# Kernel tuning notes

Measured on AMD Instinct MI355X. Metric: run time of the kernel, lower is better.

## Reference

```python
import jax, jax.numpy as jnp
import numpy as np

P = 2  # sampling ratio: keep top ceil(M/p) measurements


def setup_inputs() -> dict:
    key = jax.random.key(0)
    k1, k2, k3 = jax.random.split(key, 3)
    B, H, W, C = 8, 1024, 1024, 3
    Y = jax.random.normal(k1, (B, H, W, C), dtype=jnp.float32)
    # build()-time Z0 components: abs ~ N(0.5, 0.1), angle ~ N(0, 0.5*sqrt(pi))
    Z0_abs = 0.5 + 0.1 * jax.random.normal(k2, (1, 1, H, W), dtype=jnp.float32)
    Z0_angle = (0.5 * np.pi ** 0.5) * jax.random.normal(k3, (1, 1, H, W), dtype=jnp.float32)
    return {"Y": Y, "Z0_abs": Z0_abs, "Z0_angle": Z0_angle}


def _make_Z0(Z0_abs, Z0_angle):
    # Z0 = |Z0| * exp(i*angle), Frobenius-normalized over spatial axes (2,3)
    Z0 = Z0_abs.astype(jnp.complex64) * jnp.exp(1j * Z0_angle.astype(jnp.complex64))
    fro = jnp.sqrt(jnp.sum(jnp.abs(Z0) ** 2, axis=(2, 3), keepdims=True)).astype(jnp.complex64)
    return Z0 / fro


def reference(Y, Z0_abs, Z0_angle):
    B, H, W, C = Y.shape
    M = H * W * C
    R = int(np.ceil(M / P))
    # transpose NHWC -> NCHW, scale by original S[2] (= W)
    Y_S = jnp.transpose(Y.astype(jnp.float32), (0, 3, 1, 2)) / jnp.float32(W)
    y_s = Y_S.reshape(B, M)
    # threshold = R-th largest value per batch (== descending-sorted index R-1)
    thr = jax.lax.top_k(y_s, R)[0][:, -1]  # [B]
    Ytr = (Y_S >= thr[:, None, None, None]).astype(jnp.float32)  # [B,C,H,W]
    Z0 = _make_Z0(Z0_abs, Z0_angle)
    return Ytr, Z0
```

## Files before the change

kernel.cpp:

```cpp
#include <hip/hip_runtime.h>
#include <math.h>

#define BATCH 8
#define HH 1024
#define WW 1024
#define CC 3
#define MTOT (HH*WW*CC)
#define RSEL 1572864u

#define WCAP 131072u
#define LCAP 1024u
#define P1B  2048
#define QPT  4

#define U_HI 0xBC800000u
#define U_LO 0x437FFFFFu

typedef float nfloat4 __attribute__((ext_vector_type(4)));
typedef float nfloat2 __attribute__((ext_vector_type(2)));

#define WS_WCNT_OFF  0u
#define WS_CHI_OFF   512u
#define WS_NPART_OFF 1024u
#define WS_THR_OFF   2048u
#define WS_FB_OFF    2112u
#define WS_NORM_OFF  2176u
#define WS_WU_OFF    4096u
#define WS_WP_OFF    4198400u

#define NCOPY 3
#define HSTRIDE 4097

__device__ __forceinline__ unsigned int fmap(float x) {
    unsigned int b = __float_as_uint(x);
    return (b & 0x80000000u) ? ~b : (b | 0x80000000u);
}

__device__ __forceinline__ void nt_store4(float4 v, float4* p) {
    nfloat4 t; t.x = v.x; t.y = v.y; t.z = v.z; t.w = v.w;
    __builtin_nontemporal_store(t, (nfloat4*)p);
}
__device__ __forceinline__ void nt_store2(float2 v, float2* p) {
    nfloat2 t; t.x = v.x; t.y = v.y;
    __builtin_nontemporal_store(t, (nfloat2*)p);
}

__device__ __forceinline__ void thresh_row_quad(const float* __restrict__ Yb,
                                                float* __restrict__ outb,
                                                int h, int w4, unsigned int tu) {
    const float4* src = (const float4*)(Yb + ((size_t)h * WW + (size_t)w4 * 4) * CC);
    float4 a0 = src[0], a1 = src[1], a2 = src[2];
    float4 r0, r1, r2;
    r0.x = (fmap(a0.x) >= tu) ? 1.f : 0.f;
    r0.y = (fmap(a0.w) >= tu) ? 1.f : 0.f;
    r0.z = (fmap(a1.z) >= tu) ? 1.f : 0.f;
    r0.w = (fmap(a2.y) >= tu) ? 1.f : 0.f;
    r1.x = (fmap(a0.y) >= tu) ? 1.f : 0.f;
    r1.y = (fmap(a1.x) >= tu) ? 1.f : 0.f;
    r1.z = (fmap(a1.w) >= tu) ? 1.f : 0.f;
    r1.w = (fmap(a2.z) >= tu) ? 1.f : 0.f;
    r2.x = (fmap(a0.z) >= tu) ? 1.f : 0.f;
    r2.y = (fmap(a1.y) >= tu) ? 1.f : 0.f;
    r2.z = (fmap(a2.x) >= tu) ? 1.f : 0.f;
    r2.w = (fmap(a2.w) >= tu) ? 1.f : 0.f;
    size_t base = (size_t)h * WW;
    ((float4*)(outb + base))[w4]                        = r0;
    ((float4*)(outb + base + (size_t)HH * WW))[w4]      = r1;
    ((float4*)(outb + base + (size_t)2 * HH * WW))[w4]  = r2;
}

__global__ void __launch_bounds__(256, 4) pass1_kernel(
                             const float* __restrict__ Y,
                             const float* __restrict__ zabs,
                             float* __restrict__ out,
                             unsigned int* __restrict__ wu,
                             unsigned int* __restrict__ wpos,
                             unsigned int* __restrict__ wcnt,
                             unsigned int* __restrict__ chib,
                             float* __restrict__ npart) {
    const int tid = threadIdx.x;

    if (blockIdx.x >= P1B) {
        const int bx = blockIdx.x - P1B;
        float s = 0.f;
        const int n4z = HH * WW / 4;
        for (int i = bx * 256 + tid; i < n4z; i += 256 * 256) {
            float4 v = ((const float4*)zabs)[i];
            s += v.x * v.x + v.y * v.y + v.z * v.z + v.w * v.w;
        }
        for (int d = 32; d > 0; d >>= 1) s += __shfl_down(s, d);
        __shared__ float ls[4];
        if ((tid & 63) == 0) ls[tid >> 6] = s;
        __syncthreads();
        if (tid == 0) npart[bx] = ls[0] + ls[1] + ls[2] + ls[3];
        return;
    }

    __shared__ unsigned int lu[LCAP];
    __shared__ unsigned int lp[LCAP];
    __shared__ unsigned int lcnt;
    __shared__ unsigned int red[4];
    __shared__ unsigned int gbase_s;
    if (tid == 0) lcnt = 0u;
    __syncthreads();

    const int blk = blockIdx.x;
    const int b = blk >> 8;
    const int p0 = (blk & 255) * 1024 + tid;
    const float* Yb = Y + (size_t)b * MTOT;
    float* outb = out + (size_t)b * MTOT;
    float4* o4 = (float4*)outb;

    float4 A0[QPT], A1[QPT], A2[QPT];
#pragma unroll
    for (int it = 0; it < QPT; it++) {
        int p = p0 + it * 256;
        const float4* src = (const float4*)(Yb + (size_t)p * 12);
        A0[it] = src[0]; A1[it] = src[1]; A2[it] = src[2];
    }
    __builtin_amdgcn_sched_barrier(0);

    unsigned int hcnt = 0u;
    unsigned long long wmask = 0ull;

#pragma unroll
    for (int it = 0; it < QPT; it++) {
        const int p = p0 + it * 256;
        float4 a0 = A0[it], a1 = A1[it], a2 = A2[it];
        float4 r0, r1, r2;

#define CLS(val, dst, j) do { \
        unsigned int u = fmap(val); \
        bool hi = (u >= U_HI); \
        dst = hi ? 1.f : 0.f; \
        hcnt += hi ? 1u : 0u; \
        if (!hi && u >= U_LO) wmask |= (1ull << (it * 12 + (j))); \
    } while (0)

        CLS(a0.x, r0.x, 0); CLS(a0.w, r0.y, 1); CLS(a1.z, r0.z, 2); CLS(a2.y, r0.w, 3);
        CLS(a0.y, r1.x, 4); CLS(a1.x, r1.y, 5); CLS(a1.w, r1.z, 6); CLS(a2.z, r1.w, 7);
        CLS(a0.z, r2.x, 8); CLS(a1.y, r2.y, 9); CLS(a2.x, r2.z, 10); CLS(a2.w, r2.w, 11);
#undef CLS

        nt_store4(r0, &o4[p]);
        nt_store4(r1, &o4[262144 + p]);
        nt_store4(r2, &o4[524288 + p]);
    }

    if (wmask) {
        unsigned int nw = (unsigned int)__popcll(wmask);
        unsigned int base = atomicAdd(&lcnt, nw);
#pragma unroll
        for (int it = 0; it < QPT; it++) {
            const int p = p0 + it * 256;
            const unsigned int rb = (unsigned int)(4 * p);
            float4 a0 = A0[it], a1 = A1[it], a2 = A2[it];
#define EMIT(val, ch, k, j) do { \
            if (wmask & (1ull << (it * 12 + (j)))) { \
                if (base < LCAP) { lu[base] = fmap(val); lp[base] = (unsigned int)((ch) * HH * WW) + rb + (k); } \
                base++; \
            } \
        } while (0)
            EMIT(a0.x, 0, 0, 0); EMIT(a0.w, 0, 1, 1); EMIT(a1.z, 0, 2, 2); EMIT(a2.y, 0, 3, 3);
            EMIT(a0.y, 1, 0, 4); EMIT(a1.x, 1, 1, 5); EMIT(a1.w, 1, 2, 6); EMIT(a2.z, 1, 3, 7);
            EMIT(a0.z, 2, 0, 8); EMIT(a1.y, 2, 1, 9); EMIT(a2.x, 2, 2, 10); EMIT(a2.w, 2, 3, 11);
#undef EMIT
        }
    }

    __syncthreads();
    unsigned int n = lcnt;
    unsigned int nc = (n > LCAP) ? LCAP : n;
    if (tid == 0) {
        unsigned int add = (n > LCAP) ? (WCAP + 1u) : n;
        gbase_s = atomicAdd(&wcnt[b * 16], add);
    }
    for (int d = 32; d > 0; d >>= 1) hcnt += __shfl_down(hcnt, d);
    if ((tid & 63) == 0) red[tid >> 6] = hcnt;
    __syncthreads();
    if (tid == 0) atomicAdd(&chib[b * 16], red[0] + red[1] + red[2] + red[3]);

    unsigned int gbase = gbase_s;
    unsigned int* wub = wu + (size_t)b * WCAP;
    unsigned int* wpb = wpos + (size_t)b * WCAP;
    for (unsigned int j = tid; j < nc; j += 256u) {
        unsigned int q = gbase + j;
        if (q < WCAP) { wub[q] = lu[j]; wpb[q] = lp[j]; }
    }
}

__global__ void __launch_bounds__(1024) refine_kernel(
        const float* __restrict__ Y,
        const unsigned int* __restrict__ wu,
        const unsigned int* __restrict__ wcnt,
        const unsigned int* __restrict__ chib,
        const float* __restrict__ npart,
        unsigned int* __restrict__ thr,
        unsigned int* __restrict__ fbflag,
        float* __restrict__ normsum) {
    const int tid = threadIdx.x;

    if (blockIdx.x == 8) {
        float s = (tid < 256) ? npart[tid] : 0.f;
        for (int d = 32; d > 0; d >>= 1) s += __shfl_down(s, d);
        __shared__ float ls[16];
        if ((tid & 63) == 0) ls[tid >> 6] = s;
        __syncthreads();
        if (tid == 0) {
            float t = 0.f;
            for (int i = 0; i < 16; i++) t += ls[i];
            *normsum = t;
        }
        return;
    }

    __shared__ unsigned int hist[NCOPY * HSTRIDE];
    __shared__ unsigned int waveSums[16];
    __shared__ unsigned int selBin, selBase;
    const int b = blockIdx.x;
    const int lane = tid & 63, wid = tid >> 6;
    const int hc = (wid % NCOPY) * HSTRIDE;

    const unsigned int wc = wcnt[b * 16];
    const unsigned int Ch = chib[b * 16];
    const int fb = (wc > WCAP) || (Ch >= RSEL) || (Ch + wc < RSEL);
    unsigned int target = fb ? RSEL : (RSEL - Ch);
    const unsigned int wcg = (wc > WCAP) ? WCAP : wc;
    const unsigned int* wp = wu + (size_t)b * WCAP;
    const float* Yb = Y + (size_t)b * MTOT;

    unsigned int d1 = 0, d2 = 0;

    for (int level = 0; level < 3; level++) {
        const int nb  = (level < 2) ? 4096 : 256;
        const int bpt = (level < 2) ? 4 : 1;
        for (int i = tid; i < NCOPY * HSTRIDE; i += 1024) hist[i] = 0u;
        if (tid == 0) { selBin = 0u; selBase = 0u; }
        __syncthreads();

#define HISTO(u) do { \
            if (level == 0) atomicAdd(&hist[hc + ((u) >> 20)], 1u); \
            else if (level == 1) { if (((u) >> 20) == d1) atomicAdd(&hist[hc + (((u) >> 8) & 0xFFFu)], 1u); } \
            else { if (((u) >> 8) == ((d1 << 12) | d2)) atomicAdd(&hist[hc + ((u) & 0xFFu)], 1u); } \
        } while (0)

        if (fb) {
            for (unsigned int i = tid; i < (unsigned int)MTOT; i += 1024u) {
                unsigned int u = fmap(Yb[i]);
                HISTO(u);
            }
        } else {
            for (unsigned int i = tid; i < wcg; i += 1024u) {
                unsigned int u = wp[i];
                HISTO(u);
            }
        }
#undef HISTO
        __syncthreads();
        unsigned int c[4] = {0u, 0u, 0u, 0u};
        unsigned int s = 0u;
        const int nthr = nb / bpt;
        if (tid < nthr)
            for (int k = 0; k < bpt; k++) {
                int bin = nb - 1 - (tid * bpt + k);
                c[k] = hist[bin] + hist[HSTRIDE + bin] + hist[2 * HSTRIDE + bin];
                s += c[k];
            }
        unsigned int incl = s;
        for (int d = 1; d < 64; d <<= 1) {
            unsigned int v = __shfl_up(incl, d);
            if (lane >= d) incl += v;
        }
        if (lane == 63) waveSums[wid] = incl;
        __syncthreads();
        if (tid < 16) {
            unsigned int w = waveSums[tid];
            for (int d = 1; d < 16; d <<= 1) {
                unsigned int v = __shfl_up(w, d);
                if (tid >= d) w += v;
            }
            waveSums[tid] = w;
        }
        __syncthreads();
        incl += (wid > 0) ? waveSums[wid - 1] : 0u;
        unsigned int excl = incl - s;
        if (s > 0u && excl < target && incl >= target) {
            unsigned int run = excl;
            for (int k = 0; k < bpt; k++) {
                if (run + c[k] >= target) {
                    selBin = (unsigned int)(nb - 1 - (tid * bpt + k));
                    selBase = run;
                    break;
                }
                run += c[k];
            }
        }
        __syncthreads();
        if (level == 0) d1 = selBin;
        else if (level == 1) d2 = selBin;
        target -= selBase;
        __syncthreads();
    }
    if (tid == 0) {
        thr[b] = (d1 << 20) | (d2 << 8) | selBin;
        fbflag[b] = (unsigned int)fb;
    }
}

__global__ void fixup_z_kernel(const float* __restrict__ Y,
                               const unsigned int* __restrict__ wu,
                               const unsigned int* __restrict__ wpos,
                               const unsigned int* __restrict__ wcnt,
                               const unsigned int* __restrict__ thr,
                               const unsigned int* __restrict__ fbflag,
                               const float* __restrict__ zabs,
                               const float* __restrict__ zang,
                               const float* __restrict__ normsum,
                               float* __restrict__ out,
                               float* __restrict__ outz, int interleaved) {
    const int tid = threadIdx.x;
    if (blockIdx.x < 2048) {
        int i = blockIdx.x * 256 + tid;
        float inv = 1.0f / sqrtf(*normsum);
        float2 a = ((const float2*)zabs)[i];
        float2 g = ((const float2*)zang)[i];
        float s0, c0, s1, c1;
        __sincosf(g.x, &s0, &c0);
        __sincosf(g.y, &s1, &c1);
        if (interleaved) {
            float4 o;
            o.x = a.x * c0 * inv; o.y = a.x * s0 * inv;
            o.z = a.y * c1 * inv; o.w = a.y * s1 * inv;
            nt_store4(o, &((float4*)outz)[i]);
        } else {
            float2 o;
            o.x = a.x * c0 * inv; o.y = a.y * c1 * inv;
            nt_store2(o, &((float2*)outz)[i]);
        }
    } else {
        const int j = blockIdx.x - 2048;
        const int b = j >> 8;
        const unsigned int tu = thr[b];
        float* outb = out + (size_t)b * MTOT;
        if (fbflag[b]) {
            const float* Yb = Y + (size_t)b * MTOT;
            for (int q = (j & 255); q < 1024; q += 256) {
                int pq = q * 256 + tid;
                thresh_row_quad(Yb, outb, pq >> 8, pq & 255, tu);
            }
        } else {
            const unsigned int wc = wcnt[b * 16];
            const unsigned int* wub = wu + (size_t)b * WCAP;
            const unsigned int* wpb = wpos + (size_t)b * WCAP;
            for (unsigned int i = (unsigned int)(j & 255) * 256u + tid; i < wc; i += 65536u) {
                unsigned int u = wub[i];
                unsigned int pos = wpb[i];
                outb[pos] = (u >= tu) ? 1.f : 0.f;
            }
        }
    }
}

extern "C" void kernel_launch(void* const* d_in, const int* in_sizes, int n_in,
                              void* d_out, int out_size, void* d_ws, size_t ws_size,
                              hipStream_t stream) {
    const float* Y    = (const float*)d_in[0];
    const float* zabs = (const float*)d_in[1];
    const float* zang = (const float*)d_in[2];
    float* out = (float*)d_out;

    unsigned char* ws = (unsigned char*)d_ws;
    unsigned int* wcnt  = (unsigned int*)(ws + WS_WCNT_OFF);
    unsigned int* chib  = (unsigned int*)(ws + WS_CHI_OFF);
    float*        npart = (float*)(ws + WS_NPART_OFF);
    unsigned int* thr   = (unsigned int*)(ws + WS_THR_OFF);
    unsigned int* fbf   = (unsigned int*)(ws + WS_FB_OFF);
    float*        norm  = (float*)(ws + WS_NORM_OFF);
    unsigned int* wu    = (unsigned int*)(ws + WS_WU_OFF);
    unsigned int* wpos  = (unsigned int*)(ws + WS_WP_OFF);

    (void)hipMemsetAsync(ws, 0, 1024, stream);

    pass1_kernel<<<P1B + 256, 256, 0, stream>>>(Y, zabs, out, wu, wpos, wcnt, chib, npart);
    refine_kernel<<<9, 1024, 0, stream>>>(Y, wu, wcnt, chib, npart, thr, fbf, norm);

    size_t zoff = (size_t)BATCH * CC * HH * WW;
    int zfloats = out_size - (int)zoff;
    int interleaved = (zfloats >= 2 * HH * WW) ? 1 : 0;
    fixup_z_kernel<<<2048 + 2048, 256, 0, stream>>>(
        Y, wu, wpos, wcnt, thr, fbf, zabs, zang, norm, out, out + zoff, interleaved);
}
```

Baseline: 256.9 us.

## Fuse Z0 generation into refine kernel and shrink fixup grid

Moves the Z0 complex-normalisation work into the refine launch as 512 extra 1024-thread blocks, so it overlaps the 8 single-block histogram refinements instead of running in the fixup kernel. Each Z block recomputes the norm reduction itself, which removes the separate normsum write and read. The fixup kernel drops from 2048 scatter blocks to 256 blocks with strided loops. Nontemporal stores are replaced by ordinary stores in pass1 and the Z output. The risks are a weaker fallback path now that fixup has far fewer blocks, and cache pollution from the regular stores.

```diff
diff --git a/kernel.cpp b/kernel.cpp
--- a/kernel.cpp
+++ b/kernel.cpp
@@ -16,15 +16,11 @@
 #define U_HI 0xBC800000u
 #define U_LO 0x437FFFFFu
 
-typedef float nfloat4 __attribute__((ext_vector_type(4)));
-typedef float nfloat2 __attribute__((ext_vector_type(2)));
-
 #define WS_WCNT_OFF  0u
 #define WS_CHI_OFF   512u
 #define WS_NPART_OFF 1024u
 #define WS_THR_OFF   2048u
 #define WS_FB_OFF    2112u
-#define WS_NORM_OFF  2176u
 #define WS_WU_OFF    4096u
 #define WS_WP_OFF    4198400u
 
@@ -34,15 +30,6 @@
 __device__ __forceinline__ unsigned int fmap(float x) {
     unsigned int b = __float_as_uint(x);
     return (b & 0x80000000u) ? ~b : (b | 0x80000000u);
-}
-
-__device__ __forceinline__ void nt_store4(float4 v, float4* p) {
-    nfloat4 t; t.x = v.x; t.y = v.y; t.z = v.z; t.w = v.w;
-    __builtin_nontemporal_store(t, (nfloat4*)p);
-}
-__device__ __forceinline__ void nt_store2(float2 v, float2* p) {
-    nfloat2 t; t.x = v.x; t.y = v.y;
-    __builtin_nontemporal_store(t, (nfloat2*)p);
 }
 
 __device__ __forceinline__ void thresh_row_quad(const float* __restrict__ Yb,
@@ -142,9 +129,9 @@
         CLS(a0.z, r2.x, 8); CLS(a1.y, r2.y, 9); CLS(a2.x, r2.z, 10); CLS(a2.w, r2.w, 11);
 #undef CLS
 
-        nt_store4(r0, &o4[p]);
-        nt_store4(r1, &o4[262144 + p]);
-        nt_store4(r2, &o4[524288 + p]);
+        o4[p]           = r0;
+        o4[262144 + p]  = r1;
+        o4[524288 + p]  = r2;
     }
 
     if (wmask) {
@@ -197,19 +184,34 @@
         const float* __restrict__ npart,
         unsigned int* __restrict__ thr,
         unsigned int* __restrict__ fbflag,
-        float* __restrict__ normsum) {
+        const float* __restrict__ zabs,
+        const float* __restrict__ zang,
+        float* __restrict__ outz, int interleaved) {
     const int tid = threadIdx.x;
 
-    if (blockIdx.x == 8) {
+    if (blockIdx.x >= 8) {
+        const int z = blockIdx.x - 8;
+        __shared__ float ls[4];
         float s = (tid < 256) ? npart[tid] : 0.f;
         for (int d = 32; d > 0; d >>= 1) s += __shfl_down(s, d);
-        __shared__ float ls[16];
-        if ((tid & 63) == 0) ls[tid >> 6] = s;
-        __syncthreads();
-        if (tid == 0) {
-            float t = 0.f;
-            for (int i = 0; i < 16; i++) t += ls[i];
-            *normsum = t;
+        if (tid < 256 && (tid & 63) == 0) ls[tid >> 6] = s;
+        __syncthreads();
+        float inv = 1.0f / sqrtf(ls[0] + ls[1] + ls[2] + ls[3]);
+        int i = z * 1024 + tid;
+        float2 a = ((const float2*)zabs)[i];
+        float2 g = ((const float2*)zang)[i];
+        float s0, c0, s1, c1;
+        __sincosf(g.x, &s0, &c0);
+        __sincosf(g.y, &s1, &c1);
+        if (interleaved) {
+            float4 o;
+            o.x = a.x * c0 * inv; o.y = a.x * s0 * inv;
+            o.z = a.y * c1 * inv; o.w = a.y * s1 * inv;
+            ((float4*)outz)[i] = o;
+        } else {
+            float2 o;
+            o.x = a.x * c0 * inv; o.y = a.y * c1 * inv;
+            ((float2*)outz)[i] = o;
         }
         return;
     }
@@ -307,56 +309,29 @@
     }
 }
 
-__global__ void fixup_z_kernel(const float* __restrict__ Y,
-                               const unsigned int* __restrict__ wu,
-                               const unsigned int* __restrict__ wpos,
-                               const unsigned int* __restrict__ wcnt,
-                               const unsigned int* __restrict__ thr,
-                               const unsigned int* __restrict__ fbflag,
-                               const float* __restrict__ zabs,
-                               const float* __restrict__ zang,
-                               const float* __restrict__ normsum,
-                               float* __restrict__ out,
-                               float* __restrict__ outz, int interleaved) {
+__global__ void fixup_kernel(const float* __restrict__ Y,
+                             const unsigned int* __restrict__ wu,
+                             const unsigned int* __restrict__ wpos,
+                             const unsigned int* __restrict__ wcnt,
+                             const unsigned int* __restrict__ thr,
+                             const unsigned int* __restrict__ fbflag,
+                             float* __restrict__ out) {
     const int tid = threadIdx.x;
-    if (blockIdx.x < 2048) {
-        int i = blockIdx.x * 256 + tid;
-        float inv = 1.0f / sqrtf(*normsum);
-        float2 a = ((const float2*)zabs)[i];
-        float2 g = ((const float2*)zang)[i];
-        float s0, c0, s1, c1;
-        __sincosf(g.x, &s0, &c0);
-        __sincosf(g.y, &s1, &c1);
-        if (interleaved) {
-            float4 o;
-            o.x = a.x * c0 * inv; o.y = a.x * s0 * inv;
-            o.z = a.y * c1 * inv; o.w = a.y * s1 * inv;
-            nt_store4(o, &((float4*)outz)[i]);
-        } else {
-            float2 o;
-            o.x = a.x * c0 * inv; o.y = a.y * c1 * inv;
-            nt_store2(o, &((float2*)outz)[i]);
+    const int j = blockIdx.x;
+    const int b = j >> 5;
+    const unsigned int tu = thr[b];
+    float* outb = out + (size_t)b * MTOT;
+    if (fbflag[b]) {
+        const float* Yb = Y + (size_t)b * MTOT;
+        for (int q = (j & 31) * 256 + tid; q < 262144; q += 8192) {
+            thresh_row_quad(Yb, outb, q >> 8, q & 255, tu);
         }
     } else {
-        const int j = blockIdx.x - 2048;
-        const int b = j >> 8;
-        const unsigned int tu = thr[b];
-        float* outb = out + (size_t)b * MTOT;
-        if (fbflag[b]) {
-            const float* Yb = Y + (size_t)b * MTOT;
-            for (int q = (j & 255); q < 1024; q += 256) {
-                int pq = q * 256 + tid;
-                thresh_row_quad(Yb, outb, pq >> 8, pq & 255, tu);
-            }
-        } else {
-            const unsigned int wc = wcnt[b * 16];
-            const unsigned int* wub = wu + (size_t)b * WCAP;
-            const unsigned int* wpb = wpos + (size_t)b * WCAP;
-            for (unsigned int i = (unsigned int)(j & 255) * 256u + tid; i < wc; i += 65536u) {
-                unsigned int u = wub[i];
-                unsigned int pos = wpb[i];
-                outb[pos] = (u >= tu) ? 1.f : 0.f;
-            }
+        const unsigned int wc = wcnt[b * 16];
+        const unsigned int* wub = wu + (size_t)b * WCAP;
+        const unsigned int* wpb = wpos + (size_t)b * WCAP;
+        for (unsigned int i = (unsigned int)(j & 31) * 256u + tid; i < wc; i += 8192u) {
+            outb[wpb[i]] = (wub[i] >= tu) ? 1.f : 0.f;
         }
     }
 }
@@ -375,18 +350,19 @@
     float*        npart = (float*)(ws + WS_NPART_OFF);
     unsigned int* thr   = (unsigned int*)(ws + WS_THR_OFF);
     unsigned int* fbf   = (unsigned int*)(ws + WS_FB_OFF);
-    float*        norm  = (float*)(ws + WS_NORM_OFF);
     unsigned int* wu    = (unsigned int*)(ws + WS_WU_OFF);
     unsigned int* wpos  = (unsigned int*)(ws + WS_WP_OFF);
 
     (void)hipMemsetAsync(ws, 0, 1024, stream);
 
     pass1_kernel<<<P1B + 256, 256, 0, stream>>>(Y, zabs, out, wu, wpos, wcnt, chib, npart);
-    refine_kernel<<<9, 1024, 0, stream>>>(Y, wu, wcnt, chib, npart, thr, fbf, norm);
 
     size_t zoff = (size_t)BATCH * CC * HH * WW;
     int zfloats = out_size - (int)zoff;
     int interleaved = (zfloats >= 2 * HH * WW) ? 1 : 0;
-    fixup_z_kernel<<<2048 + 2048, 256, 0, stream>>>(
-        Y, wu, wpos, wcnt, thr, fbf, zabs, zang, norm, out, out + zoff, interleaved);
-}
+
+    refine_kernel<<<8 + 512, 1024, 0, stream>>>(
+        Y, wu, wcnt, chib, npart, thr, fbf, zabs, zang, out + zoff, interleaved);
+
+    fixup_kernel<<<256, 256, 0, stream>>>(Y, wu, wpos, wcnt, thr, fbf, out);
+}
```

Measured after the change: 244.6 us. 4.8% less time.
